# Optimization experiments

Measured on AMD Instinct MI355X. Metric: run time of the kernel, lower is better.

## Reference

```python
import jax, jax.numpy as jnp
import numpy as np

B, D, N, M, R, C = 512, 16, 64, 32, 32, 10  # batch, divisions, feat_in, feat_map, TR-rank, categories


def setup_inputs() -> dict:
    key = jax.random.key(0)
    k1, k2, k3, k4 = jax.random.split(key, 4)
    tensor = jax.random.normal(k1, (B, D, N), dtype=jnp.float32)
    W_fm = jax.random.normal(k2, (N, M), dtype=jnp.float32) / np.sqrt(N)
    b_fm = jax.random.normal(k3, (M,), dtype=jnp.float32) * 0.01
    # one [R, M, R] tensor-ring core per (category, division)
    G = jax.random.normal(k4, (C, D, R, M, R), dtype=jnp.float32) / np.sqrt(M * R)
    return {"tensor": tensor, "W_fm": W_fm, "b_fm": b_fm, "G": G}


def reference(tensor, W_fm, b_fm, G):
    # FeatureMap: learned linear n -> m applied per division  [B, D, M]
    feat = jnp.einsum('bdn,nm->bdm', tensor, W_fm) + b_fm
    # CoreKernelTensorRing per (category, division): [B,M] x [R,M,R] -> [B,R,R]
    cores = jnp.einsum('bdm,cdimj->cdbij', feat, G)  # [C, D, B, R, R]
    # __foward_products: chained batched matmul along divisions (structural loop, D fixed)
    prod = cores[:, 0]  # [C, B, R, R]
    for d in range(1, D):
        prod = jnp.matmul(prod, cores[:, d])
    # __calculate_traces: per-sample trace, one logit per category
    logits = jnp.einsum('cbii->bc', prod)  # [B, C]
    return jax.nn.log_softmax(logits, axis=1)
```

## Files before the change

### kernel.cpp

```cpp
#include <hip/hip_runtime.h>
#include <math.h>

#define BB 512
#define DD 16
#define NN 64
#define MM 32
#define RR 32
#define CC 10
#define BBLK 8
#define ROWH 40
#define BREGH 1304

typedef _Float16 v8h __attribute__((ext_vector_type(8)));
typedef float v4f __attribute__((ext_vector_type(4)));

union H8 { unsigned int u[4]; v8h h; _Float16 e[8]; };
union H4 { unsigned int u[2]; _Float16 e[4]; };

__global__ void produce_kernel(const float* __restrict__ tensor,
                               const float* __restrict__ W,
                               const float* __restrict__ bias,
                               const float* __restrict__ G,
                               _Float16* __restrict__ fh,
                               _Float16* __restrict__ gh) {
    if (blockIdx.x < 1024) {
        int t  = blockIdx.x * 256 + threadIdx.x;
        int m  = t & (MM - 1);
        int bd = t >> 5;
        const float* tp = tensor + bd * NN;
        float acc = bias[m];
#pragma unroll
        for (int n = 0; n < NN; ++n) acc += tp[n] * W[n * MM + m];
        fh[t] = (_Float16)acc;
    } else {
        int gid  = (blockIdx.x - 1024) * 256 + threadIdx.x;
        int l    = gid & 63;
        int tile = (gid >> 6) & 63;
        int d    = (gid >> 12) & 15;
        int c    = gid >> 16;
        int i    = tile >> 1;
        int jj   = 16 * (tile & 1) + (l & 15);
        int q    = l >> 4;
        const float* src = G + ((((size_t)c * DD + d) * RR + i) * MM + 8 * q) * RR + jj;
        H8 v;
#pragma unroll
        for (int r = 0; r < 8; ++r)
            v.e[r] = (_Float16)src[(size_t)r * RR];
        *(v8h*)(gh + (size_t)gid * 8) = v.h;
    }
}

__global__ __launch_bounds__(512, 4) void chain_kernel(
    const _Float16* __restrict__ feat_h,
    const _Float16* __restrict__ g_h,
    float* __restrict__ logits)
{
    __shared__ __align__(16) _Float16 lds[BBLK * BREGH];

    const int bid  = blockIdx.x;
    const int c    = bid >> 6;
    const int b0   = (bid & 63) * BBLK;
    const int t    = threadIdx.x;
    const int w    = t >> 6;
    const int lane = t & 63;
    const int q    = lane >> 4;
    const int j4   = lane & 15;

    const size_t gbase_c = (size_t)c * DD * 32768;
    const int bA = b0 + (j4 & 7);

    v8h afh = *(const v8h*)(feat_h + (size_t)bA * (DD * MM) + 0 * MM + q * 8);
    v8h gf[8];
#pragma unroll
    for (int u = 0; u < 8; ++u) {
        const int tile = w * 8 + u;
        gf[u] = *(const v8h*)(g_h + gbase_c + ((size_t)tile * 64 + lane) * 8);
    }

    v8h pah[2];
    v4f acc[2][2];

    for (int d = 0; d < DD; ++d) {
        __syncthreads();
        v4f av[8];
#pragma unroll
        for (int u = 0; u < 8; ++u) {
            v4f z = {0.f, 0.f, 0.f, 0.f};
            av[u] = __builtin_amdgcn_mfma_f32_16x16x32_f16(afh, gf[u], z, 0, 0, 0);
        }
        if (d < DD - 1) {
            afh = *(const v8h*)(feat_h + (size_t)bA * (DD * MM) + (d + 1) * MM + q * 8);
            const size_t gb = gbase_c + (size_t)(d + 1) * 32768;
#pragma unroll
            for (int u = 0; u < 8; ++u) {
                const int tile = w * 8 + u;
                gf[u] = *(const v8h*)(g_h + gb + ((size_t)tile * 64 + lane) * 8);
            }
        }
        if (q < 2) {
#pragma unroll
            for (int jh = 0; jh < 2; ++jh)
#pragma unroll
                for (int reg = 0; reg < 4; ++reg) {
                    H4 hv;
                    hv.e[0] = (_Float16)av[0 * 2 + jh][reg];
                    hv.e[1] = (_Float16)av[1 * 2 + jh][reg];
                    hv.e[2] = (_Float16)av[2 * 2 + jh][reg];
                    hv.e[3] = (_Float16)av[3 * 2 + jh][reg];
                    *reinterpret_cast<uint2*>(
                        &lds[(4 * q + reg) * BREGH + (16 * jh + j4) * ROWH + 4 * w]) =
                        make_uint2(hv.u[0], hv.u[1]);
                }
        }
        __syncthreads();
        _Float16* base = lds + w * BREGH;
        if (d == 0) {
#pragma unroll
            for (int mi = 0; mi < 2; ++mi) {
                H8 a;
#pragma unroll
                for (int r = 0; r < 8; ++r)
                    a.e[r] = base[(8 * q + r) * ROWH + 16 * mi + j4];
                pah[mi] = a.h;
            }
        } else {
            v8h bf[2];
#pragma unroll
            for (int ni = 0; ni < 2; ++ni)
                bf[ni] = *(const v8h*)(base + (16 * ni + j4) * ROWH + 8 * q);
#pragma unroll
            for (int mi = 0; mi < 2; ++mi)
#pragma unroll
                for (int ni = 0; ni < 2; ++ni) {
                    v4f z = {0.f, 0.f, 0.f, 0.f};
                    acc[mi][ni] = __builtin_amdgcn_mfma_f32_16x16x32_f16(
                        pah[mi], bf[ni], z, 0, 0, 0);
                }
            if (d < DD - 1) {
#pragma unroll
                for (int mi = 0; mi < 2; ++mi)
#pragma unroll
                    for (int ni = 0; ni < 2; ++ni)
#pragma unroll
                        for (int reg = 0; reg < 4; ++reg)
                            base[(16 * mi + 4 * q + reg) * ROWH + 16 * ni + j4] =
                                (_Float16)acc[mi][ni][reg];
                __builtin_amdgcn_sched_barrier(0);
#pragma unroll
                for (int mi = 0; mi < 2; ++mi)
                    pah[mi] = *(const v8h*)(base + (16 * mi + j4) * ROWH + 8 * q);
            }
        }
    }

    float tr = 0.f;
    if (q == (j4 >> 2)) {
        int reg = j4 & 3;
        tr = acc[0][0][reg] + acc[1][1][reg];
    }
#pragma unroll
    for (int off = 32; off > 0; off >>= 1) tr += __shfl_down(tr, off);
    if (lane == 0) logits[(b0 + w) * CC + c] = tr;
}

__global__ void lsm_kernel(const float* __restrict__ logits,
                           float* __restrict__ out) {
    int b = blockIdx.x * blockDim.x + threadIdx.x;
    if (b >= BB) return;
    float x[CC];
    float mx = -1e30f;
#pragma unroll
    for (int c = 0; c < CC; ++c) { x[c] = logits[b * CC + c]; mx = fmaxf(mx, x[c]); }
    float s = 0.f;
#pragma unroll
    for (int c = 0; c < CC; ++c) s += expf(x[c] - mx);
    float ls = logf(s);
#pragma unroll
    for (int c = 0; c < CC; ++c) out[b * CC + c] = x[c] - mx - ls;
}

extern "C" void kernel_launch(void* const* d_in, const int* in_sizes, int n_in,
                              void* d_out, int out_size, void* d_ws, size_t ws_size,
                              hipStream_t stream) {
    const float* tensor = (const float*)d_in[0];
    const float* W      = (const float*)d_in[1];
    const float* bias   = (const float*)d_in[2];
    const float* G      = (const float*)d_in[3];
    float* out = (float*)d_out;

    const size_t FEAT = (size_t)BB * DD * MM;
    const size_t GPK  = (size_t)CC * DD * 64 * 64 * 8;
    _Float16* fh = (_Float16*)d_ws;
    _Float16* gh = fh + FEAT;
    float* logits = (float*)(gh + GPK);

    produce_kernel<<<1024 + (int)(GPK / 8 / 256), 256, 0, stream>>>(
        tensor, W, bias, G, fh, gh);
    chain_kernel<<<CC * (BB / BBLK), 512, 0, stream>>>(fh, gh, logits);
    lsm_kernel<<<(BB + 255) / 256, 256, 0, stream>>>(logits, out);
}
```

Before: 125.1 us.

## Stage produce inputs in LDS with coalesced loads and remap chain blocks per XCD

The feature-map half of produce_kernel now stages its tensor rows and the whole W matrix in shared memory before the dot products. The G-packing half now reads G with coalesced float4 loads, converts to fp16 in LDS, then writes the MFMA-ready tile layout. This replaces the old strided scalar reads. Chain blocks are remapped so each category's blocks land on the same XCD (by blockIdx modulo 8), to improve L2 reuse of that category's G cores. The costs are LDS use and an extra barrier in produce_kernel, plus uneven XCD load for categories 8 and 9.

Measured after the change: 124.1 us. About the same (-0.8%).

```diff
diff --git a/kernel.cpp b/kernel.cpp
--- a/kernel.cpp
+++ b/kernel.cpp
@@ -17,36 +17,58 @@
 union H8 { unsigned int u[4]; v8h h; _Float16 e[8]; };
 union H4 { unsigned int u[2]; _Float16 e[4]; };
 
-__global__ void produce_kernel(const float* __restrict__ tensor,
-                               const float* __restrict__ W,
-                               const float* __restrict__ bias,
-                               const float* __restrict__ G,
-                               _Float16* __restrict__ fh,
-                               _Float16* __restrict__ gh) {
+__global__ __launch_bounds__(256) void produce_kernel(
+    const float* __restrict__ tensor, const float* __restrict__ W,
+    const float* __restrict__ bias,   const float* __restrict__ G,
+    _Float16* __restrict__ fh,        _Float16* __restrict__ gh) {
+    __shared__ __align__(16) char smem[36864];
+    const int t = threadIdx.x;
     if (blockIdx.x < 1024) {
-        int t  = blockIdx.x * 256 + threadIdx.x;
-        int m  = t & (MM - 1);
-        int bd = t >> 5;
-        const float* tp = tensor + bd * NN;
+        float* ten_s = (float*)smem;
+        float* W_s   = (float*)smem + 512;
+        const int bd0 = blockIdx.x * 8;
+        if (t < 128)
+            *(float4*)(ten_s + t * 4) = *(const float4*)(tensor + bd0 * NN + t * 4);
+        *(float4*)(W_s + t * 4)        = *(const float4*)(W + t * 4);
+        *(float4*)(W_s + 1024 + t * 4) = *(const float4*)(W + 1024 + t * 4);
+        __syncthreads();
+        const int m = t & 31, bd_l = t >> 5;
         float acc = bias[m];
 #pragma unroll
-        for (int n = 0; n < NN; ++n) acc += tp[n] * W[n * MM + m];
-        fh[t] = (_Float16)acc;
+        for (int n = 0; n < NN; ++n) acc += ten_s[bd_l * NN + n] * W_s[n * MM + m];
+        fh[(bd0 + bd_l) * MM + m] = (_Float16)acc;
     } else {
-        int gid  = (blockIdx.x - 1024) * 256 + threadIdx.x;
-        int l    = gid & 63;
-        int tile = (gid >> 6) & 63;
-        int d    = (gid >> 12) & 15;
-        int c    = gid >> 16;
-        int i    = tile >> 1;
-        int jj   = 16 * (tile & 1) + (l & 15);
-        int q    = l >> 4;
-        const float* src = G + ((((size_t)c * DD + d) * RR + i) * MM + 8 * q) * RR + jj;
-        H8 v;
-#pragma unroll
-        for (int r = 0; r < 8; ++r)
-            v.e[r] = (_Float16)src[(size_t)r * RR];
-        *(v8h*)(gh + (size_t)gid * 8) = v.h;
+        _Float16* lg = (_Float16*)smem;
+        const int pb = blockIdx.x - 1024;
+        const int c  = pb >> 5;
+        const int d  = (pb >> 1) & 15;
+        const int hf = pb & 1;
+        const float* src = G + (size_t)(c * DD + d) * 32768 + hf * 16384;
+#pragma unroll
+        for (int k = 0; k < 16; ++k) {
+            const int f = (k * 256 + t) * 4;
+            float4 v = *(const float4*)(src + f);
+            const int di = f >> 10, m = (f >> 5) & 31, j = f & 31;
+            H4 hv;
+            hv.e[0] = (_Float16)v.x; hv.e[1] = (_Float16)v.y;
+            hv.e[2] = (_Float16)v.z; hv.e[3] = (_Float16)v.w;
+            *(uint2*)(lg + di * 1152 + m * 36 + j) = make_uint2(hv.u[0], hv.u[1]);
+        }
+        __syncthreads();
+#pragma unroll
+        for (int k = 0; k < 8; ++k) {
+            const int idx = k * 256 + t;
+            const int tl = idx >> 6, ln = idx & 63;
+            const int di = tl >> 1;
+            const int q = ln >> 4, j4 = ln & 15;
+            const int j = (tl & 1) * 16 + j4;
+            H8 o;
+#pragma unroll
+            for (int r = 0; r < 8; ++r)
+                o.e[r] = lg[di * 1152 + (8 * q + r) * 36 + j];
+            const size_t gi = ((size_t)(c * DD + d) * 64 + hf * 32 + tl) * 64 + ln;
+            *(v8h*)(gh + gi * 8) = o.h;
+        }
     }
 }
 
@@ -57,9 +79,18 @@
 {
     __shared__ __align__(16) _Float16 lds[BBLK * BREGH];
 
-    const int bid  = blockIdx.x;
-    const int c    = bid >> 6;
-    const int b0   = (bid & 63) * BBLK;
+    const int bid = blockIdx.x;
+    const int xcd = bid & 7;
+    const int idx = bid >> 3;
+    int c, sub;
+    if (idx < 64) { c = xcd; sub = idx; }
+    else {
+        const int e = idx - 64;
+        if (xcd < 4) { c = 8; sub = xcd * 16 + e; }
+        else         { c = 9; sub = (xcd - 4) * 16 + e; }
+    }
+    const int b0 = sub * BBLK;
+
     const int t    = threadIdx.x;
     const int w    = t >> 6;
     const int lane = t & 63;
@@ -69,13 +100,11 @@
     const size_t gbase_c = (size_t)c * DD * 32768;
     const int bA = b0 + (j4 & 7);
 
-    v8h afh = *(const v8h*)(feat_h + (size_t)bA * (DD * MM) + 0 * MM + q * 8);
+    v8h afh = *(const v8h*)(feat_h + (size_t)bA * (DD * MM) + q * 8);
     v8h gf[8];
 #pragma unroll
-    for (int u = 0; u < 8; ++u) {
-        const int tile = w * 8 + u;
-        gf[u] = *(const v8h*)(g_h + gbase_c + ((size_t)tile * 64 + lane) * 8);
-    }
+    for (int u = 0; u < 8; ++u)
+        gf[u] = *(const v8h*)(g_h + gbase_c + ((size_t)(w * 8 + u) * 64 + lane) * 8);
 
     v8h pah[2];
     v4f acc[2][2];
@@ -92,10 +121,8 @@
             afh = *(const v8h*)(feat_h + (size_t)bA * (DD * MM) + (d + 1) * MM + q * 8);
             const size_t gb = gbase_c + (size_t)(d + 1) * 32768;
 #pragma unroll
-            for (int u = 0; u < 8; ++u) {
-                const int tile = w * 8 + u;
-                gf[u] = *(const v8h*)(g_h + gb + ((size_t)tile * 64 + lane) * 8);
-            }
+            for (int u = 0; u < 8; ++u)
+                gf[u] = *(const v8h*)(g_h + gb + ((size_t)(w * 8 + u) * 64 + lane) * 8);
         }
         if (q < 2) {
 #pragma unroll
@@ -103,10 +130,10 @@
 #pragma unroll
                 for (int reg = 0; reg < 4; ++reg) {
                     H4 hv;
-                    hv.e[0] = (_Float16)av[0 * 2 + jh][reg];
-                    hv.e[1] = (_Float16)av[1 * 2 + jh][reg];
-                    hv.e[2] = (_Float16)av[2 * 2 + jh][reg];
-                    hv.e[3] = (_Float16)av[3 * 2 + jh][reg];
+                    hv.e[0] = (_Float16)av[0 + jh][reg];
+                    hv.e[1] = (_Float16)av[2 + jh][reg];
+                    hv.e[2] = (_Float16)av[4 + jh][reg];
+                    hv.e[3] = (_Float16)av[6 + jh][reg];
                     *reinterpret_cast<uint2*>(
                         &lds[(4 * q + reg) * BREGH + (16 * jh + j4) * ROWH + 4 * w]) =
                         make_uint2(hv.u[0], hv.u[1]);
@@ -194,8 +221,7 @@
     _Float16* gh = fh + FEAT;
     float* logits = (float*)(gh + GPK);
 
-    produce_kernel<<<1024 + (int)(GPK / 8 / 256), 256, 0, stream>>>(
-        tensor, W, bias, G, fh, gh);
+    produce_kernel<<<1024 + 320, 256, 0, stream>>>(tensor, W, bias, G, fh, gh);
     chain_kernel<<<CC * (BB / BBLK), 512, 0, stream>>>(fh, gh, logits);
     lsm_kernel<<<(BB + 255) / 256, 256, 0, stream>>>(logits, out);
 }
```
